# Performance work log

Hardware: AMD Instinct MI355X
Metric: run time of the kernel (lower is better)

Reference implementation:

```python
import jax, jax.numpy as jnp
import numpy as np

N_E = 1024      # codebook_emb_num
E_DIM = 512     # codebook_emb_dim
BETA = 0.25


def setup_inputs() -> dict:
    key = jax.random.key(0)
    k1, k2 = jax.random.split(key)
    z = jax.random.normal(k1, (16, E_DIM, 64, 64), dtype=jnp.float32)
    # nn.Embedding default init: N(0,1)
    codebook = jax.random.normal(k2, (N_E, E_DIM), dtype=jnp.float32)
    return {"z": z, "codebook": codebook}


def reference(z, codebook):
    b, c, h, w = z.shape
    # (B,C,H,W) -> (B,H,W,C) -> (N, e_dim)
    z_p = jnp.transpose(z, (0, 2, 3, 1))
    z_flat = z_p.reshape(-1, c)

    d = (jnp.sum(z_flat * z_flat, axis=1, keepdims=True)
         + jnp.sum(codebook * codebook, axis=1)
         - 2.0 * z_flat @ codebook.T)

    idx = jnp.argmin(d, axis=1)                       # [N]
    # one-hot @ codebook is mathematically a gather
    z_q = codebook[idx].reshape(z_p.shape)            # [B,H,W,C]

    sg = jax.lax.stop_gradient
    e_latent_loss = jnp.mean((sg(z_q) - z_p) ** 2)
    q_latent_loss = jnp.mean((z_q - sg(z_p)) ** 2)
    codebook_loss = q_latent_loss + e_latent_loss * BETA

    # straight-through estimator
    z_q_st = z_p + sg(z_q - z_p)
    z_q_out = jnp.transpose(z_q_st, (0, 3, 1, 2))     # back to (B,C,H,W)
    indices = idx.reshape(b, 1, h, w)
    return z_q_out, codebook_loss, indices
```

## Files before the change

### kernel.cpp

```cpp
#include <hip/hip_runtime.h>

#define N_E   1024
#define E_DIM 512
#define HW_   4096
#define NVEC  65536
#define ZQ_ELEMS 33554432
#define BETA 0.25f
#define DELTA 384.0f

typedef _Float16 half8 __attribute__((ext_vector_type(8), aligned(16)));
typedef float f32x4 __attribute__((ext_vector_type(4)));
typedef unsigned int u32x4 __attribute__((ext_vector_type(4), aligned(16)));

union H16 { _Float16 f; unsigned short u; };

__device__ __forceinline__ float PK(float d, int j) {
    return __int_as_float((__float_as_int(d) & ~1023) | j);
}

#define GLDS(gp, lp) __builtin_amdgcn_global_load_lds( \
    (const __attribute__((address_space(1))) void*)(gp), \
    (__attribute__((address_space(3))) void*)(lp), 16, 0, 0)

__global__ __launch_bounds__(64) void vq_prep(const float* __restrict__ cb,
    float* __restrict__ ynorm) {
    int j = blockIdx.x, l = threadIdx.x;
    float s = 0.f;
    for (int i = 0; i < 8; ++i) {
        float v = cb[(j << 9) + l + (i << 6)];
        s += v * v;
    }
#pragma unroll
    for (int off = 32; off > 0; off >>= 1) s += __shfl_xor(s, off);
    if (l == 0) ynorm[j] = s * 1024.f;
}

__global__ __launch_bounds__(256) void vq_prepB(const float* __restrict__ cb,
    unsigned short* __restrict__ Bf) {
    int j16 = blockIdx.x;
    int t = threadIdx.x;
#pragma unroll
    for (int s = 0; s < 4; ++s) {
        int G = ((s << 8) + t) << 3;
        int c = G >> 9, w = G & 511;
        int lane = w >> 3;
        int j = (j16 << 4) + (lane & 15);
        int k0 = (c << 5) + ((lane >> 4) << 3);
        const float* p = cb + ((long)j << 9) + k0;
        unsigned short o8[8];
#pragma unroll
        for (int e = 0; e < 8; ++e) {
            H16 hh; hh.f = (_Float16)(32.f * p[e]);
            o8[e] = hh.u;
        }
        *(u32x4*)&Bf[((long)j16 << 13) + G] = *(u32x4*)&o8[0];
    }
}

__global__ __launch_bounds__(256) void vq_pack(const float* __restrict__ z,
    unsigned short* __restrict__ Ah,
    float* __restrict__ zpart, int base_b, int bid0) {
    __shared__ float T[64][65];
    __shared__ float ps[4];
    int bid = blockIdx.x;
    int hw0 = (bid & 63) << 6;
    int c0 = ((bid >> 6) & 7) << 6;
    int bb = (bid >> 9) + base_b;
    int t = threadIdx.x;
    int hl = t & 63, cl = t >> 6;
    const float* zp = z + ((long)((bb << 9) + c0 + cl)) * 4096 + hw0 + hl;
#pragma unroll
    for (int i = 0; i < 16; ++i)
        T[cl + 4 * i][hl] = zp[(long)(4 * i) * 4096];
    __syncthreads();
    int hr = t >> 2, cg = (t & 3) << 4;
    long m = ((long)(bb - base_b) << 12) + hw0 + hr;
    unsigned short h8[16];
    float s = 0.f;
#pragma unroll
    for (int e = 0; e < 16; ++e) {
        float v0 = T[cg + e][hr];
        s += v0 * v0;
        H16 hh; hh.f = (_Float16)(32.f * v0);
        h8[e] = hh.u;
    }
    long o = m * 512 + c0 + cg;
    *(u32x4*)&Ah[o]     = *(u32x4*)&h8[0];
    *(u32x4*)&Ah[o + 8] = *(u32x4*)&h8[8];
#pragma unroll
    for (int off = 32; off > 0; off >>= 1) s += __shfl_xor(s, off);
    if ((t & 63) == 0) ps[t >> 6] = s;
    __syncthreads();
    if (t == 0) zpart[bid0 + bid] = ps[0] + ps[1] + ps[2] + ps[3];
}

__global__ __launch_bounds__(256, 4) void vq_dist(
    const unsigned short* __restrict__ Ah, const unsigned short* __restrict__ Bf,
    const float* __restrict__ ynorm, int* __restrict__ ws_idx,
    float* __restrict__ out_idx, float* __restrict__ bd1g,
    float* __restrict__ bd2g, int* __restrict__ bj2g, int mbase) {

    __shared__ _Float16 sA[2][64][64];
    __shared__ float b1k[256], b2k[256];

    const int t = threadIdx.x;
    const int l = t & 63, wid = t >> 6;
    const int lid = l & 15, kg = l >> 4;
    const int m0 = blockIdx.x << 6;

    const int r8 = l >> 3, sl = l & 7, st = sl ^ r8;
    const unsigned short* gpA0 = Ah + ((long)(m0 + (wid << 3) + r8) << 9)
                                    + ((st & 4) << 3) + ((st & 3) << 3);

    auto STAGE = [&](int buf, int cpair) {
        const long ao = (long)cpair << 6;
#pragma unroll
        for (int g = 0; g < 2; ++g)
            GLDS(gpA0 + ao + ((long)g << 14), &sA[buf][(wid + (g << 2)) << 3][0]);
    };

    f32x4 acc[4][4];
    auto ZERO = [&]() {
#pragma unroll
        for (int mt = 0; mt < 4; ++mt)
#pragma unroll
            for (int jt = 0; jt < 4; ++jt) acc[mt][jt] = {0.f, 0.f, 0.f, 0.f};
    };

    auto COMPUTE = [&](int buf, int sub, int c, int p) {
        half8 ah[4];
        const int q0 = sub << 2;
#pragma unroll
        for (int mt = 0; mt < 4; ++mt) {
            int row = (mt << 4) + lid;
            ah[mt] = *(const half8*)&sA[buf][row][((q0 + kg) ^ (row & 7)) << 3];
        }
        long fb = (((long)(((p << 4) + (wid << 2)) << 4) + c) << 9) + (l << 3);
        const unsigned short* bp = Bf + fb;
#pragma unroll
        for (int jt = 0; jt < 4; ++jt) {
            half8 bh = *(const half8*)(bp);
            bp += 8192;
#pragma unroll
            for (int mt = 0; mt < 4; ++mt)
                acc[mt][jt] = __builtin_amdgcn_mfma_f32_16x16x32_f16(ah[mt], bh, acc[mt][jt], 0, 0, 0);
        }
    };

    auto FOLD = [&](int p) {
        const int jgb = (p << 8) + (wid << 6);
        float yn[4]; int jg[4];
#pragma unroll
        for (int jt = 0; jt < 4; ++jt) {
            jg[jt] = jgb + (jt << 4) + lid;
            yn[jt] = ynorm[jg[jt]];
        }
#pragma unroll
        for (int mt = 0; mt < 4; ++mt)
#pragma unroll
            for (int r = 0; r < 4; ++r) {
                float k0 = PK(yn[0] - 2.f * acc[mt][0][r], jg[0]);
                float k1 = PK(yn[1] - 2.f * acc[mt][1][r], jg[1]);
                float k2 = PK(yn[2] - 2.f * acc[mt][2][r], jg[2]);
                float k3 = PK(yn[3] - 2.f * acc[mt][3][r], jg[3]);
                float m1 = fminf(k0, k1), M1 = fmaxf(k0, k1);
                float m2 = fminf(k2, k3), M2 = fmaxf(k2, k3);
                float best = fminf(m1, m2);
                float sec  = fminf(fmaxf(m1, m2), fminf(M1, M2));
#pragma unroll
                for (int off = 1; off < 16; off <<= 1) {
                    float e1 = __shfl_xor(best, off);
                    float e2 = __shfl_xor(sec, off);
                    sec  = fminf(fminf(sec, e2), fmaxf(best, e1));
                    best = fminf(best, e1);
                }
                if (lid == 0) {
                    int slot = (((mt << 4) + (kg << 2) + r) << 2) + wid;
                    float B1 = b1k[slot], B2 = b2k[slot];
                    b2k[slot] = fminf(fminf(B2, sec), fmaxf(B1, best));
                    b1k[slot] = fminf(B1, best);
                }
            }
    };

    b1k[t] = 3.4e38f; b2k[t] = 3.4e38f;
    ZERO();
    STAGE(0, 0);
    __syncthreads();

    int buf = 0;
    for (int cp = 0; cp < 32; ++cp) {
        int p = cp >> 3, pc = cp & 7;
        if (cp < 31) STAGE(buf ^ 1, (cp + 1) & 7);
        COMPUTE(buf, 0, (pc << 1),     p);
        COMPUTE(buf, 1, (pc << 1) + 1, p);
        if (pc == 7) { FOLD(p); ZERO(); }
        __syncthreads();
        buf ^= 1;
    }

    if (t < 64) {
        float K1 = 3.4e38f, K2 = 3.4e38f;
#pragma unroll
        for (int w2 = 0; w2 < 4; ++w2) {
            int slot = (t << 2) + w2;
            float e1 = b1k[slot], e2 = b2k[slot];
            K2 = fminf(fminf(K2, e2), fmaxf(K1, e1));
            K1 = fminf(K1, e1);
        }
        int m = mbase + m0 + t;
        int u1 = __float_as_int(K1), u2 = __float_as_int(K2);
        int J1 = u1 & 1023, J2 = u2 & 1023;
        ws_idx[m]  = J1;
        out_idx[m] = (float)J1;
        bd1g[m] = __int_as_float(u1 & ~1023);
        bd2g[m] = __int_as_float(u2 & ~1023);
        bj2g[m] = J2;
    }
}

__global__ __launch_bounds__(256) void vq_refine(const float* __restrict__ z,
    const float* __restrict__ cb, const float* __restrict__ ynorm,
    const float* __restrict__ bd2, const int* __restrict__ bj2,
    int* __restrict__ ws_idx, float* __restrict__ out_idx, float* __restrict__ bd1) {
    int l = threadIdx.x & 63;
    int wv = (blockIdx.x << 2) + (threadIdx.x >> 6);
    for (int m = wv; m < NVEC; m += 4096) {
        float d1 = bd1[m];
        if (bd2[m] - d1 > DELTA) continue;
        int j1 = ws_idx[m], j2 = bj2[m];
        const float* zr = z + ((long)(m >> 12) << 21) + (m & 4095);
        const float* c1 = cb + ((long)j1 << 9);
        const float* c2 = cb + ((long)j2 << 9);
        float s1 = 0.f, s2 = 0.f;
#pragma unroll
        for (int e = 0; e < 8; ++e) {
            int c = (l << 3) + e;
            float a = zr[(long)c << 12];
            s1 = fmaf(a, c1[c], s1);
            s2 = fmaf(a, c2[c], s2);
        }
#pragma unroll
        for (int off = 32; off > 0; off >>= 1) {
            s1 += __shfl_xor(s1, off);
            s2 += __shfl_xor(s2, off);
        }
        float de1 = ynorm[j1] - 2048.f * s1;
        float de2 = ynorm[j2] - 2048.f * s2;
        bool take2 = de2 < de1 || (de2 == de1 && j2 < j1);
        if (l == 0) {
            if (take2) { ws_idx[m] = j2; out_idx[m] = (float)j2; bd1[m] = de2; }
            else       { bd1[m] = de1; }
        }
    }
}

__global__ __launch_bounds__(256) void vq_gather(const float* __restrict__ cb,
    const int* __restrict__ ws_idx, float* __restrict__ out) {
    int base = blockIdx.x * 256 + threadIdx.x;
    int hw  = base & 4095;
    int c4g = (base >> 12) & 31;
    int b   = base >> 17;
    int j   = ws_idx[(b << 12) | hw];
#pragma unroll
    for (int it = 0; it < 4; ++it) {
        int c4 = (c4g << 2) + it;
        float4 v = ((const float4*)cb)[(j << 7) + c4];
        long zo = ((long)((b << 9) + (c4 << 2))) * 4096 + hw;
        out[zo] = v.x; out[zo + 4096] = v.y; out[zo + 8192] = v.z; out[zo + 12288] = v.w;
    }
}

__global__ __launch_bounds__(1024) void vq_final(const float* __restrict__ bd1,
    const float* __restrict__ zpart, float* __restrict__ out) {
    int t = threadIdx.x;
    double s = 0.0;
#pragma unroll
    for (int i = 0; i < 64; ++i) s += (double)bd1[t + (i << 10)];
    s *= (1.0 / 1024.0);
#pragma unroll
    for (int i = 0; i < 8; ++i) s += (double)zpart[t + (i << 10)];
#pragma unroll
    for (int off = 32; off > 0; off >>= 1) s += __shfl_xor(s, off);
    __shared__ double pd[16];
    if ((t & 63) == 0) pd[t >> 6] = s;
    __syncthreads();
    if (t == 0) {
        double tot = 0.0;
#pragma unroll
        for (int i = 0; i < 16; ++i) tot += pd[i];
        out[ZQ_ELEMS] = (float)(1.25 * tot / 33554432.0);
    }
}

extern "C" void kernel_launch(void* const* d_in, const int* in_sizes, int n_in,
                              void* d_out, int out_size, void* d_ws, size_t ws_size,
                              hipStream_t stream) {
    const float* z  = (const float*)d_in[0];
    const float* cb = (const float*)d_in[1];
    float* out = (float*)d_out;
    char* ws = (char*)d_ws;

    float* ynorm = (float*)(ws + 1024);
    int*   ws_idx = (int*)(ws + 8192);
    float* bd1   = (float*)(ws + 272 * 1024);
    float* bd2   = (float*)(ws + 528 * 1024);
    int*   bj2   = (int*)(ws + 784 * 1024);
    float* zpart = (float*)(ws + 1040 * 1024);
    unsigned short* Bf = (unsigned short*)(ws + (2L << 20));
    const size_t base = 4L << 20;
    unsigned short* Ah = (unsigned short*)(ws + base);

    int nphase = 1;
    while (nphase < 16) {
        size_t Asz = (size_t)(65536 / nphase) * 512 * 2;
        if (base + Asz <= ws_size) break;
        nphase <<= 1;
    }

    vq_prep<<<N_E, 64, 0, stream>>>(cb, ynorm);
    vq_prepB<<<64, 256, 0, stream>>>(cb, Bf);
    int PM = 65536 / nphase;
    for (int p = 0; p < nphase; ++p) {
        vq_pack<<<8192 / nphase, 256, 0, stream>>>(z, Ah, zpart,
                                                   p * (16 / nphase),
                                                   p * (8192 / nphase));
        vq_dist<<<PM / 64, 256, 0, stream>>>(Ah, Bf, ynorm, ws_idx,
                                             out + ZQ_ELEMS + 1, bd1, bd2, bj2, p * PM);
    }
    vq_refine<<<1024, 256, 0, stream>>>(z, cb, ynorm, bd2, bj2, ws_idx,
                                        out + ZQ_ELEMS + 1, bd1);
    vq_gather<<<NVEC / 256 * 32, 256, 0, stream>>>(cb, ws_idx, out);
    vq_final<<<1, 1024, 0, stream>>>(bd1, zpart, out);
}
```

Measured before the change: 192.3 us.

## Double vq_dist block to 128 rows, fuse codebook norm into prepB, drop zeroing

The distance kernel now runs 512 threads per block covering 128 rows instead of 64. The two row-halves of waves share each codebook B fragment load pattern, and the A staging tile doubles. The separate ynorm kernel is folded into vq_prepB to save one launch. Accumulator zeroing is replaced by passing a zero C operand on the first MFMA of each pass. The cost is larger LDS use and fewer blocks, which may lower occupancy.

```diff
diff --git a/kernel.cpp b/kernel.cpp
--- a/kernel.cpp
+++ b/kernel.cpp
@@ -22,21 +22,8 @@
     (const __attribute__((address_space(1))) void*)(gp), \
     (__attribute__((address_space(3))) void*)(lp), 16, 0, 0)
 
-__global__ __launch_bounds__(64) void vq_prep(const float* __restrict__ cb,
-    float* __restrict__ ynorm) {
-    int j = blockIdx.x, l = threadIdx.x;
-    float s = 0.f;
-    for (int i = 0; i < 8; ++i) {
-        float v = cb[(j << 9) + l + (i << 6)];
-        s += v * v;
-    }
-#pragma unroll
-    for (int off = 32; off > 0; off >>= 1) s += __shfl_xor(s, off);
-    if (l == 0) ynorm[j] = s * 1024.f;
-}
-
 __global__ __launch_bounds__(256) void vq_prepB(const float* __restrict__ cb,
-    unsigned short* __restrict__ Bf) {
+    unsigned short* __restrict__ Bf, float* __restrict__ ynorm) {
     int j16 = blockIdx.x;
     int t = threadIdx.x;
 #pragma unroll
@@ -55,6 +42,17 @@
         }
         *(u32x4*)&Bf[((long)j16 << 13) + G] = *(u32x4*)&o8[0];
     }
+    int jloc = t >> 4, sub = t & 15;
+    int j = (j16 << 4) + jloc;
+    float s = 0.f;
+#pragma unroll
+    for (int i = 0; i < 32; ++i) {
+        float v = cb[((long)j << 9) + (i << 4) + sub];
+        s += v * v;
+    }
+#pragma unroll
+    for (int off = 8; off > 0; off >>= 1) s += __shfl_xor(s, off);
+    if (sub == 0) ynorm[j] = s * 1024.f;
 }
 
 __global__ __launch_bounds__(256) void vq_pack(const float* __restrict__ z,
@@ -94,19 +92,21 @@
     if (t == 0) zpart[bid0 + bid] = ps[0] + ps[1] + ps[2] + ps[3];
 }
 
-__global__ __launch_bounds__(256, 4) void vq_dist(
+__global__ __launch_bounds__(512, 4) void vq_dist(
     const unsigned short* __restrict__ Ah, const unsigned short* __restrict__ Bf,
     const float* __restrict__ ynorm, int* __restrict__ ws_idx,
     float* __restrict__ out_idx, float* __restrict__ bd1g,
     float* __restrict__ bd2g, int* __restrict__ bj2g, int mbase) {
 
-    __shared__ _Float16 sA[2][64][64];
-    __shared__ float b1k[256], b2k[256];
+    __shared__ _Float16 sA[2][128][64];
+    __shared__ float b1k[512], b2k[512];
 
     const int t = threadIdx.x;
     const int l = t & 63, wid = t >> 6;
     const int lid = l & 15, kg = l >> 4;
-    const int m0 = blockIdx.x << 6;
+    const int wm = (wid >> 2) << 6;
+    const int jw = wid & 3;
+    const int m0 = blockIdx.x << 7;
 
     const int r8 = l >> 3, sl = l & 7, st = sl ^ r8;
     const unsigned short* gpA0 = Ah + ((long)(m0 + (wid << 3) + r8) << 9)
@@ -116,26 +116,21 @@
         const long ao = (long)cpair << 6;
 #pragma unroll
         for (int g = 0; g < 2; ++g)
-            GLDS(gpA0 + ao + ((long)g << 14), &sA[buf][(wid + (g << 2)) << 3][0]);
+            GLDS(gpA0 + ao + ((long)g << 15), &sA[buf][(wid + (g << 3)) << 3][0]);
     };
 
     f32x4 acc[4][4];
-    auto ZERO = [&]() {
-#pragma unroll
-        for (int mt = 0; mt < 4; ++mt)
-#pragma unroll
-            for (int jt = 0; jt < 4; ++jt) acc[mt][jt] = {0.f, 0.f, 0.f, 0.f};
-    };
-
-    auto COMPUTE = [&](int buf, int sub, int c, int p) {
+    const f32x4 zc = {0.f, 0.f, 0.f, 0.f};
+
+    auto COMPUTE = [&](int buf, int sub, int c, int p, bool first) {
         half8 ah[4];
         const int q0 = sub << 2;
 #pragma unroll
         for (int mt = 0; mt < 4; ++mt) {
-            int row = (mt << 4) + lid;
+            int row = wm + (mt << 4) + lid;
             ah[mt] = *(const half8*)&sA[buf][row][((q0 + kg) ^ (row & 7)) << 3];
         }
-        long fb = (((long)(((p << 4) + (wid << 2)) << 4) + c) << 9) + (l << 3);
+        long fb = (((long)(((p << 4) + (jw << 2)) << 4) + c) << 9) + (l << 3);
         const unsigned short* bp = Bf + fb;
 #pragma unroll
         for (int jt = 0; jt < 4; ++jt) {
@@ -143,12 +138,13 @@
             bp += 8192;
 #pragma unroll
             for (int mt = 0; mt < 4; ++mt)
-                acc[mt][jt] = __builtin_amdgcn_mfma_f32_16x16x32_f16(ah[mt], bh, acc[mt][jt], 0, 0, 0);
+                acc[mt][jt] = __builtin_amdgcn_mfma_f32_16x16x32_f16(
+                    ah[mt], bh, first ? zc : acc[mt][jt], 0, 0, 0);
         }
     };
 
     auto FOLD = [&](int p) {
-        const int jgb = (p << 8) + (wid << 6);
+        const int jgb = (p << 8) + (jw << 6);
         float yn[4]; int jg[4];
 #pragma unroll
         for (int jt = 0; jt < 4; ++jt) {
@@ -175,7 +171,7 @@
                     best = fminf(best, e1);
                 }
                 if (lid == 0) {
-                    int slot = (((mt << 4) + (kg << 2) + r) << 2) + wid;
+                    int slot = ((wm + (mt << 4) + (kg << 2) + r) << 2) + jw;
                     float B1 = b1k[slot], B2 = b2k[slot];
                     b2k[slot] = fminf(fminf(B2, sec), fmaxf(B1, best));
                     b1k[slot] = fminf(B1, best);
@@ -184,7 +180,6 @@
     };
 
     b1k[t] = 3.4e38f; b2k[t] = 3.4e38f;
-    ZERO();
     STAGE(0, 0);
     __syncthreads();
 
@@ -192,14 +187,14 @@
     for (int cp = 0; cp < 32; ++cp) {
         int p = cp >> 3, pc = cp & 7;
         if (cp < 31) STAGE(buf ^ 1, (cp + 1) & 7);
-        COMPUTE(buf, 0, (pc << 1),     p);
-        COMPUTE(buf, 1, (pc << 1) + 1, p);
-        if (pc == 7) { FOLD(p); ZERO(); }
+        COMPUTE(buf, 0, (pc << 1),     p, pc == 0);
+        COMPUTE(buf, 1, (pc << 1) + 1, p, false);
+        if (pc == 7) FOLD(p);
         __syncthreads();
         buf ^= 1;
     }
 
-    if (t < 64) {
+    if (t < 128) {
         float K1 = 3.4e38f, K2 = 3.4e38f;
 #pragma unroll
         for (int w2 = 0; w2 < 4; ++w2) {
@@ -318,15 +313,14 @@
         nphase <<= 1;
     }
 
-    vq_prep<<<N_E, 64, 0, stream>>>(cb, ynorm);
-    vq_prepB<<<64, 256, 0, stream>>>(cb, Bf);
+    vq_prepB<<<64, 256, 0, stream>>>(cb, Bf, ynorm);
     int PM = 65536 / nphase;
     for (int p = 0; p < nphase; ++p) {
         vq_pack<<<8192 / nphase, 256, 0, stream>>>(z, Ah, zpart,
                                                    p * (16 / nphase),
                                                    p * (8192 / nphase));
-        vq_dist<<<PM / 64, 256, 0, stream>>>(Ah, Bf, ynorm, ws_idx,
-                                             out + ZQ_ELEMS + 1, bd1, bd2, bj2, p * PM);
+        vq_dist<<<PM / 128, 512, 0, stream>>>(Ah, Bf, ynorm, ws_idx,
+                                              out + ZQ_ELEMS + 1, bd1, bd2, bj2, p * PM);
     }
     vq_refine<<<1024, 256, 0, stream>>>(z, cb, ynorm, bd2, bj2, ws_idx,
                                         out + ZQ_ELEMS + 1, bd1);
```

Result: slower. 217.9 us (+13.3%).
